# Kernel optimization log

Measured on AMD Instinct MI355X. Metric: run time of the kernel, lower is better.

## Reference

```python
import jax, jax.numpy as jnp
import numpy as np

B, L, E, H = 2, 2048, 2048, 16
HD = E // H  # 128
ROPE_BASE = 10000.0


def setup_inputs() -> dict:
    key = jax.random.key(0)
    k1, k2, k3 = jax.random.split(key, 3)
    x = jax.random.normal(k1, (B, L, E), dtype=jnp.float32)
    position_ids = jnp.tile(jnp.arange(L, dtype=jnp.int32)[None, :], (B, 1))
    # Linear weights stored as [in, out] so y = x @ W + b (equals torch x @ W.T + b)
    W_attn = jax.random.normal(k2, (E, 3 * E), dtype=jnp.float32) * (1.0 / np.sqrt(E))
    b_attn = jnp.zeros((3 * E,), dtype=jnp.float32)
    W_proj = jax.random.normal(k3, (E, E), dtype=jnp.float32) * (1.0 / np.sqrt(E))
    b_proj = jnp.zeros((E,), dtype=jnp.float32)
    return {"x": x, "position_ids": position_ids, "W_attn": W_attn,
            "b_attn": b_attn, "W_proj": W_proj, "b_proj": b_proj}


def _rotate_half(t):
    h = t.shape[-1] // 2
    return jnp.concatenate([-t[..., h:], t[..., :h]], axis=-1)


def _apply_rope(q, k, position_ids):
    # q,k: [B,H,L,HD]; position_ids: [B,L]
    inv_freq = 1.0 / (ROPE_BASE ** (jnp.arange(0, HD, 2, dtype=jnp.float32) / HD))
    angles = position_ids.astype(jnp.float32)[:, :, None] * inv_freq  # [B,L,HD/2]
    cos = jnp.concatenate([jnp.cos(angles)] * 2, axis=-1)[:, None]  # [B,1,L,HD]
    sin = jnp.concatenate([jnp.sin(angles)] * 2, axis=-1)[:, None]
    return q * cos + _rotate_half(q) * sin, k * cos + _rotate_half(k) * sin


def reference(x, position_ids, W_attn, b_attn, W_proj, b_proj):
    # fused QKV projection
    qkv = x @ W_attn + b_attn                       # [B,L,3E]
    q, k, v = jnp.split(qkv, 3, axis=-1)            # each [B,L,E]
    reshape = lambda t: t.reshape(B, L, H, HD).transpose(0, 2, 1, 3)  # [B,H,L,HD]
    q, k, v = reshape(q), reshape(k), reshape(v)
    q, k = _apply_rope(q, k, position_ids)
    # scaled dot-product attention (mask=None -> full attention, dropout 0)
    scores = jnp.einsum('bhqd,bhkd->bhqk', q, k) * (1.0 / np.sqrt(HD))
    probs = jax.nn.softmax(scores, axis=-1)
    y = jnp.einsum('bhqk,bhkd->bhqd', probs, v)     # [B,H,L,HD]
    y = y.transpose(0, 2, 1, 3).reshape(B, L, E)
    return y @ W_proj + b_proj
```

## Files before the change

### kernel.cpp

```cpp
#include <hip/hip_runtime.h>
#include <math.h>

#define BB 2
#define LL 2048
#define EE 2048
#define HH 16
#define HD 128
#define N3E (3*EE)

typedef __attribute__((ext_vector_type(8))) short  bf16x8;
typedef __attribute__((ext_vector_type(4))) float  f32x4;

__device__ __forceinline__ ushort f2bf(float f) {
    union { float f; unsigned u; } v; v.f = f;
    unsigned u = v.u + 0x7FFFu + ((v.u >> 16) & 1u);
    return (ushort)(u >> 16);
}
__device__ __forceinline__ float bf2f(ushort u) {
    union { unsigned u; float f; } v; v.u = ((unsigned)u) << 16;
    return v.f;
}

__global__ __launch_bounds__(256) void cvt_bf16(const float* __restrict__ in,
                                                ushort* __restrict__ out, int n) {
    int i = (blockIdx.x * 256 + threadIdx.x) * 8;
    float4 a = *(const float4*)(in + i);
    float4 b = *(const float4*)(in + i + 4);
    ushort4 p0 = { f2bf(a.x), f2bf(a.y), f2bf(a.z), f2bf(a.w) };
    ushort4 p1 = { f2bf(b.x), f2bf(b.y), f2bf(b.z), f2bf(b.w) };
    *(ushort4*)(out + i)     = p0;
    *(ushort4*)(out + i + 4) = p1;
}

__global__ __launch_bounds__(256) void transpose_bf16(const float* __restrict__ in,
                                                      ushort* __restrict__ out,
                                                      int R, int Ccol) {
    __shared__ float tile[32][33];
    int c0 = blockIdx.x * 32, r0 = blockIdx.y * 32;
    int t = threadIdx.x;
    int lr = t >> 5, lc = t & 31;
    #pragma unroll
    for (int i = 0; i < 4; ++i)
        tile[lr + i * 8][lc] = in[(size_t)(r0 + lr + i * 8) * Ccol + c0 + lc];
    __syncthreads();
    #pragma unroll
    for (int i = 0; i < 4; ++i)
        out[(size_t)(c0 + lr + i * 8) * R + r0 + lc] = f2bf(tile[lc][lr + i * 8]);
}

template<int WRITE_BF16>
__global__ __launch_bounds__(512, 2) void gemm_ktile(const ushort* __restrict__ A,
                                                     const ushort* __restrict__ Bt,
                                                     const float* __restrict__ bias,
                                                     void* __restrict__ C,
                                                     int M, int N, int K, int nby) {
    __shared__ __align__(16) ushort Asl[4 * 8192];
    __shared__ __align__(16) ushort Bsl[4 * 4096];

    const int t    = threadIdx.x;
    const int lane = t & 63;
    const int w    = t >> 6;
    const int m    = lane & 15;
    const int quad = lane >> 4;
    const int wm   = w >> 1;
    const int wn   = w & 1;

    const int nwg = gridDim.x;
    const int cpx = nwg >> 3;
    const int swz = ((int)blockIdx.x & 7) * cpx + ((int)blockIdx.x >> 3);
    const int by  = swz % nby;
    const int bx  = swz / nby;
    const int m0  = by * 256, n0 = bx * 128;

    const int r16s  = (t >> 2) & 15;
    const int kels  = ((t & 3) ^ ((t & 32) ? 2 : 0)) * 8;
    const int row0s = ((t >> 6) << 4) + r16s;
    const int row1s = row0s + 128;

    const int foff = m * 32 + ((quad * 8) ^ ((m & 8) ? 16 : 0));

#define STAGE(T_) do { int _s = (T_) & 3; \
    __builtin_amdgcn_global_load_lds( \
        (const __attribute__((address_space(1))) unsigned int*)(A + (size_t)(m0 + row0s) * K + (T_) * 32 + kels), \
        (__attribute__((address_space(3))) unsigned int*)(Asl + _s * 8192 + t * 8), 16, 0, 0); \
    __builtin_amdgcn_global_load_lds( \
        (const __attribute__((address_space(1))) unsigned int*)(A + (size_t)(m0 + row1s) * K + (T_) * 32 + kels), \
        (__attribute__((address_space(3))) unsigned int*)(Asl + _s * 8192 + (512 + t) * 8), 16, 0, 0); \
    __builtin_amdgcn_global_load_lds( \
        (const __attribute__((address_space(1))) unsigned int*)(Bt + (size_t)(n0 + row0s) * K + (T_) * 32 + kels), \
        (__attribute__((address_space(3))) unsigned int*)(Bsl + _s * 4096 + t * 8), 16, 0, 0); } while (0)

    f32x4 acc[4][4];
    #pragma unroll
    for (int i = 0; i < 4; ++i)
        #pragma unroll
        for (int j = 0; j < 4; ++j) acc[i][j] = (f32x4){0.f, 0.f, 0.f, 0.f};

    const int NT = K >> 5;

    STAGE(0); STAGE(1); STAGE(2);
    asm volatile("s_waitcnt vmcnt(6)" ::: "memory");
    __builtin_amdgcn_s_barrier();

    for (int T = 0; T < NT; ++T) {
        const int slot = T & 3;
        const ushort* as = Asl + slot * 8192 + wm * 2048;
        const ushort* bs = Bsl + slot * 4096 + wn * 2048;

        bf16x8 af[4], bf[4];
        #pragma unroll
        for (int mt = 0; mt < 4; ++mt)
            af[mt] = *(const bf16x8*)(as + mt * 512 + foff);
        #pragma unroll
        for (int nt = 0; nt < 4; ++nt)
            bf[nt] = *(const bf16x8*)(bs + nt * 512 + foff);

        if (T + 3 < NT) STAGE(T + 3);

        if (T + 3 < NT)      asm volatile("s_waitcnt vmcnt(6)" ::: "memory");
        else if (T + 2 < NT) asm volatile("s_waitcnt vmcnt(3)" ::: "memory");
        else                 asm volatile("s_waitcnt vmcnt(0)" ::: "memory");
        __builtin_amdgcn_s_barrier();
        asm volatile("s_waitcnt lgkmcnt(0)" ::: "memory");
        __builtin_amdgcn_s_setprio(1);
        #pragma unroll
        for (int mt = 0; mt < 4; ++mt)
            #pragma unroll
            for (int nt = 0; nt < 4; ++nt)
                acc[mt][nt] = __builtin_amdgcn_mfma_f32_16x16x32_bf16(af[mt], bf[nt], acc[mt][nt], 0, 0, 0);
        __builtin_amdgcn_s_setprio(0);
        __builtin_amdgcn_s_barrier();
    }
#undef STAGE

    float bcol[4];
    #pragma unroll
    for (int nt = 0; nt < 4; ++nt) bcol[nt] = bias[n0 + wn * 64 + nt * 16 + m];
    #pragma unroll
    for (int mt = 0; mt < 4; ++mt) {
        #pragma unroll
        for (int nt = 0; nt < 4; ++nt) {
            #pragma unroll
            for (int r = 0; r < 4; ++r) {
                int row = m0 + wm * 64 + mt * 16 + quad * 4 + r;
                int col = n0 + wn * 64 + nt * 16 + m;
                float v = acc[mt][nt][r] + bcol[nt];
                if (WRITE_BF16) ((ushort*)C)[(size_t)row * N + col] = f2bf(v);
                else            ((float*)C)[(size_t)row * N + col] = v;
            }
        }
    }
}

__global__ __launch_bounds__(256) void prep_qk(const ushort* __restrict__ qkvb,
                                               const int* __restrict__ pos_ids,
                                               ushort* __restrict__ Qt,
                                               ushort* __restrict__ Kt) {
    const float scale = 0.08838834764831845f;
    const float nl2b = -0.20762050593046014f;
    int idx = blockIdx.x * 256 + threadIdx.x;
    int p    = idx & 15;
    int r    = (idx >> 4) & 63;
    int tile = (idx >> 10) & 31;
    int h    = (idx >> 15) & 15;
    int b    = idx >> 19;
    int c    = p ^ (r & 15);
    int l    = tile * 64 + r;
    int half = c >> 3, cl = c & 7;
    const ushort* row = qkvb + (size_t)(b * LL + l) * N3E;
    float pos = (float)pos_ids[b * LL + l];

    bf16x8 qa = *(const bf16x8*)(row + h * HD + c * 8);
    bf16x8 qb = *(const bf16x8*)(row + h * HD + (c ^ 8) * 8);
    bf16x8 ka = *(const bf16x8*)(row + EE + h * HD + c * 8);
    bf16x8 kb = *(const bf16x8*)(row + EE + h * HD + (c ^ 8) * 8);
    bf16x8 qo, ko;
    #pragma unroll
    for (int i = 0; i < 8; ++i) {
        int j = cl * 8 + i;
        float ang = pos * exp2f((float)j * nl2b);
        float s, cs;
        sincosf(ang, &s, &cs);
        float sgn = half ? s : -s;
        float q1 = bf2f((ushort)qa[i]), q2 = bf2f((ushort)qb[i]);
        float k1 = bf2f((ushort)ka[i]), k2 = bf2f((ushort)kb[i]);
        qo[i] = (short)f2bf((q1 * cs + q2 * sgn) * scale);
        ko[i] = (short)f2bf(k1 * cs + k2 * sgn);
    }
    size_t obase = ((size_t)(b * 16 + h) * 32 + tile) * 8192 + r * 128 + p * 8;
    *(bf16x8*)(Qt + obase) = qo;
    *(bf16x8*)(Kt + obase) = ko;
}

__global__ __launch_bounds__(256) void prep_v(const ushort* __restrict__ qkvb,
                                              ushort* __restrict__ Vtt) {
    int idx = blockIdx.x * 256 + threadIdx.x;
    int p    = idx & 7;
    int r    = (idx >> 3) & 127;
    int tile = (idx >> 10) & 31;
    int h    = (idx >> 15) & 15;
    int b    = idx >> 19;
    int c    = p ^ (r & 7);
    int col  = 2 * EE + h * HD + r;
    bf16x8 o;
    #pragma unroll
    for (int i = 0; i < 8; ++i) {
        int kk = tile * 64 + c * 8 + i;
        o[i] = (short)qkvb[(size_t)(b * LL + kk) * N3E + col];
    }
    *(bf16x8*)(Vtt + ((size_t)(b * 16 + h) * 32 + tile) * 8192 + r * 64 + p * 8) = o;
}

#define PSTR 68

__global__ __launch_bounds__(256, 2) void flash2(const ushort* __restrict__ Qt,
                                                 const ushort* __restrict__ Kt,
                                                 const ushort* __restrict__ Vtt,
                                                 ushort* __restrict__ y) {
    __shared__ __align__(16) ushort Ks[64 * 128];
    __shared__ __align__(16) ushort Vs[128 * 64];
    __shared__ __align__(16) ushort Ps[4 * 32 * PSTR];

    const int t    = threadIdx.x;
    const int w    = t >> 6;
    const int lane = t & 63;
    const int m    = lane & 15;
    const int quad = lane >> 4;
    const int qblk = blockIdx.x;
    const int bh   = blockIdx.y;
    const int b    = bh >> 4, h = bh & 15;

    const ushort* Qhead = Qt  + (size_t)bh * 32 * 8192;
    const ushort* Khead = Kt  + (size_t)bh * 32 * 8192;
    const ushort* Vhead = Vtt + (size_t)bh * 32 * 8192;

    bf16x8 qf[2][4];
    #pragma unroll
    for (int mt = 0; mt < 2; ++mt) {
        int rloc = w * 32 + mt * 16 + m;
        const ushort* qtile = Qhead + (size_t)(qblk * 2 + (rloc >> 6)) * 8192
                              + (rloc & 63) * 128;
        #pragma unroll
        for (int ks = 0; ks < 4; ++ks)
            qf[mt][ks] = *(const bf16x8*)(qtile + ((ks * 4 + quad) ^ m) * 8);
    }

    f32x4 oacc[2][8];
    #pragma unroll
    for (int mt = 0; mt < 2; ++mt)
        #pragma unroll
        for (int dt = 0; dt < 8; ++dt) oacc[mt][dt] = (f32x4){0.f, 0.f, 0.f, 0.f};
    float m_i[8], l_pl[8];
    #pragma unroll
    for (int s = 0; s < 8; ++s) { m_i[s] = -INFINITY; l_pl[s] = 0.f; }

    {
        const ushort* ksrc = Khead;
        #pragma unroll
        for (int i = 0; i < 4; ++i) {
            int cid = t + i * 256;
            __builtin_amdgcn_global_load_lds(
                (const __attribute__((address_space(1))) unsigned int*)(ksrc + cid * 8),
                (__attribute__((address_space(3))) unsigned int*)(Ks + cid * 8),
                16, 0, 0);
        }
    }

    for (int kt = 0; kt < 32; ++kt) {
        asm volatile("s_waitcnt vmcnt(0)\n\ts_barrier" ::: "memory");

        {
            const ushort* vsrc = Vhead + (size_t)kt * 8192;
            #pragma unroll
            for (int i = 0; i < 4; ++i) {
                int cid = t + i * 256;
                __builtin_amdgcn_global_load_lds(
                    (const __attribute__((address_space(1))) unsigned int*)(vsrc + cid * 8),
                    (__attribute__((address_space(3))) unsigned int*)(Vs + cid * 8),
                    16, 0, 0);
            }
        }

        f32x4 sacc[2][4];
        #pragma unroll
        for (int mt = 0; mt < 2; ++mt)
            #pragma unroll
            for (int nt = 0; nt < 4; ++nt) sacc[mt][nt] = (f32x4){0.f, 0.f, 0.f, 0.f};
        __builtin_amdgcn_s_setprio(1);
        #pragma unroll
        for (int ks = 0; ks < 4; ++ks) {
            #pragma unroll
            for (int nt = 0; nt < 4; ++nt) {
                bf16x8 kf = *(const bf16x8*)&Ks[(nt * 16 + m) * 128 + (((ks * 4 + quad) ^ m)) * 8];
                sacc[0][nt] = __builtin_amdgcn_mfma_f32_16x16x32_bf16(qf[0][ks], kf, sacc[0][nt], 0, 0, 0);
                sacc[1][nt] = __builtin_amdgcn_mfma_f32_16x16x32_bf16(qf[1][ks], kf, sacc[1][nt], 0, 0, 0);
            }
        }
        __builtin_amdgcn_s_setprio(0);

        float alpha_s[2][4];
        #pragma unroll
        for (int mt = 0; mt < 2; ++mt) {
            #pragma unroll
            for (int r = 0; r < 4; ++r) {
                int slot = mt * 4 + r;
                float mx = fmaxf(fmaxf(sacc[mt][0][r], sacc[mt][1][r]),
                                 fmaxf(sacc[mt][2][r], sacc[mt][3][r]));
                #pragma unroll
                for (int off = 1; off < 16; off <<= 1) mx = fmaxf(mx, __shfl_xor(mx, off, 64));
                float mnew = fmaxf(m_i[slot], mx);
                float al = __expf(m_i[slot] - mnew);
                m_i[slot] = mnew;
                float rs = 0.f;
                #pragma unroll
                for (int nt = 0; nt < 4; ++nt) {
                    float pv = __expf(sacc[mt][nt][r] - mnew);
                    sacc[mt][nt][r] = pv;
                    rs += pv;
                }
                l_pl[slot] = l_pl[slot] * al + rs;
                alpha_s[mt][r] = al;
            }
        }
        #pragma unroll
        for (int mt = 0; mt < 2; ++mt)
            #pragma unroll
            for (int dt = 0; dt < 8; ++dt)
                #pragma unroll
                for (int r = 0; r < 4; ++r) oacc[mt][dt][r] *= alpha_s[mt][r];

        #pragma unroll
        for (int mt = 0; mt < 2; ++mt)
            #pragma unroll
            for (int nt = 0; nt < 4; ++nt)
                #pragma unroll
                for (int r = 0; r < 4; ++r)
                    Ps[w * 32 * PSTR + (mt * 16 + quad * 4 + r) * PSTR + nt * 16 + m]
                        = f2bf(sacc[mt][nt][r]);

        asm volatile("s_waitcnt vmcnt(0)\n\ts_barrier" ::: "memory");

        if (kt + 1 < 32) {
            const ushort* ksrc = Khead + (size_t)(kt + 1) * 8192;
            #pragma unroll
            for (int i = 0; i < 4; ++i) {
                int cid = t + i * 256;
                __builtin_amdgcn_global_load_lds(
                    (const __attribute__((address_space(1))) unsigned int*)(ksrc + cid * 8),
                    (__attribute__((address_space(3))) unsigned int*)(Ks + cid * 8),
                    16, 0, 0);
            }
        }

        __builtin_amdgcn_s_setprio(1);
        #pragma unroll
        for (int ks2 = 0; ks2 < 2; ++ks2) {
            bf16x8 pf0 = *(const bf16x8*)&Ps[w * 32 * PSTR + (0 * 16 + m) * PSTR + ks2 * 32 + quad * 8];
            bf16x8 pf1 = *(const bf16x8*)&Ps[w * 32 * PSTR + (1 * 16 + m) * PSTR + ks2 * 32 + quad * 8];
            #pragma unroll
            for (int dt = 0; dt < 8; ++dt) {
                bf16x8 vf = *(const bf16x8*)&Vs[(dt * 16 + m) * 64 + (((ks2 * 4 + quad) ^ (m & 7))) * 8];
                oacc[0][dt] = __builtin_amdgcn_mfma_f32_16x16x32_bf16(pf0, vf, oacc[0][dt], 0, 0, 0);
                oacc[1][dt] = __builtin_amdgcn_mfma_f32_16x16x32_bf16(pf1, vf, oacc[1][dt], 0, 0, 0);
            }
        }
        __builtin_amdgcn_s_setprio(0);
    }

    #pragma unroll
    for (int s = 0; s < 8; ++s) {
        #pragma unroll
        for (int off = 1; off < 16; off <<= 1) l_pl[s] += __shfl_xor(l_pl[s], off, 64);
        l_pl[s] = 1.0f / l_pl[s];
    }
    #pragma unroll
    for (int mt = 0; mt < 2; ++mt) {
        #pragma unroll
        for (int dt = 0; dt < 8; ++dt) {
            #pragma unroll
            for (int r = 0; r < 4; ++r) {
                int row = qblk * 128 + w * 32 + mt * 16 + quad * 4 + r;
                y[(size_t)(b * LL + row) * EE + h * HD + dt * 16 + m]
                    = f2bf(oacc[mt][dt][r] * l_pl[mt * 4 + r]);
            }
        }
    }
}

extern "C" void kernel_launch(void* const* d_in, const int* in_sizes, int n_in,
                              void* d_out, int out_size, void* d_ws, size_t ws_size,
                              hipStream_t stream) {
    const float* x      = (const float*)d_in[0];
    const int*   pos    = (const int*)d_in[1];
    const float* W_attn = (const float*)d_in[2];
    const float* b_attn = (const float*)d_in[3];
    const float* W_proj = (const float*)d_in[4];
    const float* b_proj = (const float*)d_in[5];
    float* out = (float*)d_out;

    const int M = BB * LL;
    ushort* xb   = (ushort*)d_ws;
    ushort* Wat  = xb   + (size_t)M * EE;
    ushort* Wpt  = Wat  + (size_t)N3E * EE;
    ushort* qkvb = Wpt  + (size_t)EE * EE;
    ushort* Kt   = qkvb + (size_t)M * N3E;
    ushort* Vtt  = Kt   + (size_t)M * EE;
    ushort* Qt   = xb;
    ushort* yb   = Wat;

    dim3 blk(256);
    cvt_bf16<<<dim3(M * EE / (256 * 8)), blk, 0, stream>>>(x, xb, M * EE);
    transpose_bf16<<<dim3(N3E / 32, EE / 32), blk, 0, stream>>>(W_attn, Wat, EE, N3E);
    transpose_bf16<<<dim3(EE / 32, EE / 32), blk, 0, stream>>>(W_proj, Wpt, EE, EE);

    gemm_ktile<1><<<dim3((M / 256) * (N3E / 128)), dim3(512), 0, stream>>>(
        xb, Wat, b_attn, qkvb, M, N3E, EE, M / 256);

    prep_qk<<<dim3(4096), blk, 0, stream>>>(qkvb, pos, Qt, Kt);
    prep_v<<<dim3(4096), blk, 0, stream>>>(qkvb, Vtt);

    flash2<<<dim3(LL / 128, BB * HH), blk, 0, stream>>>(Qt, Kt, Vtt, yb);

    gemm_ktile<0><<<dim3((M / 256) * (EE / 128)), dim3(512), 0, stream>>>(
        yb, Wpt, b_proj, out, M, EE, EE, M / 256);
}
```

Before: 458.1 us.

## Double-buffer GEMM register fragments to overlap LDS reads with MFMA

Restructures the GEMM main loop so the LDS fragment reads for tile T+1 go into a second register set while the MFMAs for tile T run, using a ping-pong pair of register buffers and a loop unrolled by two. This aims to hide LDS read latency behind matrix instructions instead of waiting on lgkmcnt(0) before each MFMA block. It raises VGPR pressure, which may lower occupancy, and assumes NT is even. At the last iteration it also reads a stale slot, which is harmless.

```diff
diff --git a/kernel.cpp b/kernel.cpp
--- a/kernel.cpp
+++ b/kernel.cpp
@@ -90,6 +90,48 @@
         (const __attribute__((address_space(1))) unsigned int*)(Bt + (size_t)(n0 + row0s) * K + (T_) * 32 + kels), \
         (__attribute__((address_space(3))) unsigned int*)(Bsl + _s * 4096 + t * 8), 16, 0, 0); } while (0)
 
+#define GITER(T_, AU, BU, AP, BP) do { \
+    if ((T_) + 3 < NT) STAGE((T_) + 3); \
+    if ((T_) + 3 < NT)      asm volatile("s_waitcnt vmcnt(6)" ::: "memory"); \
+    else if ((T_) + 2 < NT) asm volatile("s_waitcnt vmcnt(3)" ::: "memory"); \
+    else                    asm volatile("s_waitcnt vmcnt(0)" ::: "memory"); \
+    __builtin_amdgcn_s_barrier(); \
+    asm volatile("" ::: "memory"); \
+    { \
+        const int _sl = ((T_) + 1) & 3; \
+        const ushort* _as = Asl + _sl * 8192 + wm * 2048; \
+        const ushort* _bs = Bsl + _sl * 4096 + wn * 2048; \
+        AP[0] = *(const bf16x8*)(_as + 0 * 512 + foff); \
+        AP[1] = *(const bf16x8*)(_as + 1 * 512 + foff); \
+        AP[2] = *(const bf16x8*)(_as + 2 * 512 + foff); \
+        AP[3] = *(const bf16x8*)(_as + 3 * 512 + foff); \
+        BP[0] = *(const bf16x8*)(_bs + 0 * 512 + foff); \
+        BP[1] = *(const bf16x8*)(_bs + 1 * 512 + foff); \
+        BP[2] = *(const bf16x8*)(_bs + 2 * 512 + foff); \
+        BP[3] = *(const bf16x8*)(_bs + 3 * 512 + foff); \
+    } \
+    __builtin_amdgcn_s_setprio(1); \
+    acc[0][0] = __builtin_amdgcn_mfma_f32_16x16x32_bf16(AU[0], BU[0], acc[0][0], 0, 0, 0); \
+    acc[0][1] = __builtin_amdgcn_mfma_f32_16x16x32_bf16(AU[0], BU[1], acc[0][1], 0, 0, 0); \
+    acc[0][2] = __builtin_amdgcn_mfma_f32_16x16x32_bf16(AU[0], BU[2], acc[0][2], 0, 0, 0); \
+    acc[0][3] = __builtin_amdgcn_mfma_f32_16x16x32_bf16(AU[0], BU[3], acc[0][3], 0, 0, 0); \
+    acc[1][0] = __builtin_amdgcn_mfma_f32_16x16x32_bf16(AU[1], BU[0], acc[1][0], 0, 0, 0); \
+    acc[1][1] = __builtin_amdgcn_mfma_f32_16x16x32_bf16(AU[1], BU[1], acc[1][1], 0, 0, 0); \
+    acc[1][2] = __builtin_amdgcn_mfma_f32_16x16x32_bf16(AU[1], BU[2], acc[1][2], 0, 0, 0); \
+    acc[1][3] = __builtin_amdgcn_mfma_f32_16x16x32_bf16(AU[1], BU[3], acc[1][3], 0, 0, 0); \
+    acc[2][0] = __builtin_amdgcn_mfma_f32_16x16x32_bf16(AU[2], BU[0], acc[2][0], 0, 0, 0); \
+    acc[2][1] = __builtin_amdgcn_mfma_f32_16x16x32_bf16(AU[2], BU[1], acc[2][1], 0, 0, 0); \
+    acc[2][2] = __builtin_amdgcn_mfma_f32_16x16x32_bf16(AU[2], BU[2], acc[2][2], 0, 0, 0); \
+    acc[2][3] = __builtin_amdgcn_mfma_f32_16x16x32_bf16(AU[2], BU[3], acc[2][3], 0, 0, 0); \
+    acc[3][0] = __builtin_amdgcn_mfma_f32_16x16x32_bf16(AU[3], BU[0], acc[3][0], 0, 0, 0); \
+    acc[3][1] = __builtin_amdgcn_mfma_f32_16x16x32_bf16(AU[3], BU[1], acc[3][1], 0, 0, 0); \
+    acc[3][2] = __builtin_amdgcn_mfma_f32_16x16x32_bf16(AU[3], BU[2], acc[3][2], 0, 0, 0); \
+    acc[3][3] = __builtin_amdgcn_mfma_f32_16x16x32_bf16(AU[3], BU[3], acc[3][3], 0, 0, 0); \
+    __builtin_amdgcn_s_setprio(0); \
+    asm volatile("" ::: "memory"); \
+    __builtin_amdgcn_s_barrier(); \
+} while (0)
+
     f32x4 acc[4][4];
     #pragma unroll
     for (int i = 0; i < 4; ++i)
@@ -101,36 +143,27 @@
     STAGE(0); STAGE(1); STAGE(2);
     asm volatile("s_waitcnt vmcnt(6)" ::: "memory");
     __builtin_amdgcn_s_barrier();
-
-    for (int T = 0; T < NT; ++T) {
-        const int slot = T & 3;
-        const ushort* as = Asl + slot * 8192 + wm * 2048;
-        const ushort* bs = Bsl + slot * 4096 + wn * 2048;
-
-        bf16x8 af[4], bf[4];
-        #pragma unroll
-        for (int mt = 0; mt < 4; ++mt)
-            af[mt] = *(const bf16x8*)(as + mt * 512 + foff);
-        #pragma unroll
-        for (int nt = 0; nt < 4; ++nt)
-            bf[nt] = *(const bf16x8*)(bs + nt * 512 + foff);
-
-        if (T + 3 < NT) STAGE(T + 3);
-
-        if (T + 3 < NT)      asm volatile("s_waitcnt vmcnt(6)" ::: "memory");
-        else if (T + 2 < NT) asm volatile("s_waitcnt vmcnt(3)" ::: "memory");
-        else                 asm volatile("s_waitcnt vmcnt(0)" ::: "memory");
-        __builtin_amdgcn_s_barrier();
-        asm volatile("s_waitcnt lgkmcnt(0)" ::: "memory");
-        __builtin_amdgcn_s_setprio(1);
-        #pragma unroll
-        for (int mt = 0; mt < 4; ++mt)
-            #pragma unroll
-            for (int nt = 0; nt < 4; ++nt)
-                acc[mt][nt] = __builtin_amdgcn_mfma_f32_16x16x32_bf16(af[mt], bf[nt], acc[mt][nt], 0, 0, 0);
-        __builtin_amdgcn_s_setprio(0);
-        __builtin_amdgcn_s_barrier();
-    }
+    asm volatile("" ::: "memory");
+
+    bf16x8 a0[4], b0[4], a1[4], b1[4];
+    {
+        const ushort* as = Asl + wm * 2048;
+        const ushort* bs = Bsl + wn * 2048;
+        a0[0] = *(const bf16x8*)(as + 0 * 512 + foff);
+        a0[1] = *(const bf16x8*)(as + 1 * 512 + foff);
+        a0[2] = *(const bf16x8*)(as + 2 * 512 + foff);
+        a0[3] = *(const bf16x8*)(as + 3 * 512 + foff);
+        b0[0] = *(const bf16x8*)(bs + 0 * 512 + foff);
+        b0[1] = *(const bf16x8*)(bs + 1 * 512 + foff);
+        b0[2] = *(const bf16x8*)(bs + 2 * 512 + foff);
+        b0[3] = *(const bf16x8*)(bs + 3 * 512 + foff);
+    }
+
+    for (int T = 0; T < NT; T += 2) {
+        GITER(T,     a0, b0, a1, b1);
+        GITER(T + 1, a1, b1, a0, b0);
+    }
+#undef GITER
 #undef STAGE
 
     float bcol[4];
```

New measurement: 511.2 us. +11.6%, slower.
